# Optimization experiments

Measured on AMD Instinct MI355X. Metric: run time of the kernel, lower is better.

The kernel has to match this reference:

```python
import jax, jax.numpy as jnp
import numpy as np

B, IN, HID, LAT, EH = 32768, 512, 2048, 128, 512
MID = max(HID // 2, LAT * 2)      # 1024
HALF = max(EH // 2, 4)            # 256
EPS = 1e-5
LN10 = float(np.log(10.0))


def setup_inputs() -> dict:
    key = jax.random.key(0)
    ks = jax.random.split(key, 24)
    r = lambda k, shp, s=0.02: (jax.random.normal(k, shp, dtype=jnp.float32) * s)
    d = {
        "x": jax.random.normal(ks[0], (B, IN), dtype=jnp.float32),
        "group_idx": jax.random.randint(ks[1], (B,), 0, 3),
        # encoder: Linear(IN,HID)+BN+ELU, Linear(HID,MID)+BN+ELU, Linear(MID,LAT)
        "e_w1": r(ks[2], (HID, IN)), "e_b1": jnp.zeros((HID,), jnp.float32),
        "e_g1": jnp.ones((HID,), jnp.float32), "e_be1": jnp.zeros((HID,), jnp.float32),
        "e_w2": r(ks[3], (MID, HID)), "e_b2": jnp.zeros((MID,), jnp.float32),
        "e_g2": jnp.ones((MID,), jnp.float32), "e_be2": jnp.zeros((MID,), jnp.float32),
        "e_w3": r(ks[4], (LAT, MID)), "e_b3": jnp.zeros((LAT,), jnp.float32),
        # shared: Linear(LAT+IN,HID)+BN+ELU, Linear(HID,MID)+BN+ELU
        "s_w1": r(ks[5], (HID, LAT + IN)), "s_b1": jnp.zeros((HID,), jnp.float32),
        "s_g1": jnp.ones((HID,), jnp.float32), "s_be1": jnp.zeros((HID,), jnp.float32),
        "s_w2": r(ks[6], (MID, HID)), "s_b2": jnp.zeros((MID,), jnp.float32),
        "s_g2": jnp.ones((MID,), jnp.float32), "s_be2": jnp.zeros((MID,), jnp.float32),
        # 3 expert heads, stacked on leading axis E=3
        "h_w1": r(ks[7], (3, EH, MID)), "h_b1": jnp.zeros((3, EH), jnp.float32),
        "h_w2": r(ks[8], (3, HALF, EH)), "h_b2": jnp.zeros((3, HALF), jnp.float32),
        "h_w3": r(ks[9], (3, HALF)), "h_b3": jnp.zeros((3,), jnp.float32),
    }
    return d


def _bn(h, g, b):
    # BatchNorm1d in training mode: batch mean, biased batch var
    m = jnp.mean(h, axis=0)
    v = jnp.var(h, axis=0)
    return (h - m) * (g / jnp.sqrt(v + EPS)) + b


def _elu(h):
    return jax.nn.elu(h)


def reference(x, group_idx,
              e_w1, e_b1, e_g1, e_be1, e_w2, e_b2, e_g2, e_be2, e_w3, e_b3,
              s_w1, s_b1, s_g1, s_be1, s_w2, s_b2, s_g2, s_be2,
              h_w1, h_b1, h_w2, h_b2, h_w3, h_b3):
    # encoder
    h = _elu(_bn(x @ e_w1.T + e_b1, e_g1, e_be1))
    h = _elu(_bn(h @ e_w2.T + e_b2, e_g2, e_be2))
    latent = h @ e_w3.T + e_b3                              # [B, LAT]
    # shared trunk
    z = jnp.concatenate([latent, x], axis=-1)               # [B, LAT+IN]
    h = _elu(_bn(z @ s_w1.T + s_b1, s_g1, s_be1))
    hidden = _elu(_bn(h @ s_w2.T + s_b2, s_g2, s_be2))      # [B, MID]
    # expert heads: compute all 3 (tiny vs trunk), then select per-row group
    t1 = _elu(jnp.einsum('bm,ehm->ebh', hidden, h_w1) + h_b1[:, None, :])   # [3,B,EH]
    t2 = _elu(jnp.einsum('ebh,efh->ebf', t1, h_w2) + h_b2[:, None, :])      # [3,B,HALF]
    pred_all = jnp.einsum('ebf,ef->eb', t2, h_w3) + h_b3[:, None]           # [3,B]
    pred_raw = jnp.take_along_axis(pred_all, group_idx[None, :], axis=0)[0] # [B]
    pred_log = -jax.nn.softplus(pred_raw)
    pred_prob = jnp.exp(pred_log * jnp.float32(LN10))       # 10 ** pred_log
    return pred_log, pred_prob
```

## Files before the change

### kernel.cpp

```cpp
#include <hip/hip_runtime.h>
#include <math.h>

#define B_    32768
#define LN10_ 2.302585092994046f
#define MT_H  264
#define NBLK  128

typedef __attribute__((ext_vector_type(8))) short short8;
typedef __attribute__((ext_vector_type(4))) float f32x4;

typedef const __attribute__((address_space(1))) void gvoid_t;
typedef __attribute__((address_space(3))) void svoid_t;

__device__ __forceinline__ void gl16(const void* g, void* l) {
  __builtin_amdgcn_global_load_lds((gvoid_t*)g, (svoid_t*)l, 16, 0, 0);
}

__device__ __forceinline__ float bf2f(unsigned int u) {
  union { unsigned int i; float f; } v; v.i = u << 16; return v.f;
}
__device__ __forceinline__ unsigned short f2bf(float f) {
  union { float f; unsigned int i; } v; v.f = f;
  unsigned int x = v.i;
  unsigned int r = x + 0x7FFFu + ((x >> 16) & 1u);
  return (unsigned short)(r >> 16);
}

#define HLF 8192

__global__ __launch_bounds__(512)
void gemm256(const unsigned short* __restrict__ A0_, int lda,
             const unsigned short* __restrict__ W0_, int ldw,
             unsigned short* __restrict__ C0, int ldc, int K,
             float* __restrict__ st, int Ntot) {
  __shared__ __align__(16) unsigned short lds[65536];
  const int t = threadIdx.x;
  const int nx = gridDim.x, ny = gridDim.y;
  const int f = blockIdx.y * nx + blockIdx.x;
  const int xcd = f & 7, g = f >> 3;
  const int gdiv = g / nx;
  const int mt = xcd * (ny >> 3) + gdiv;
  const int nt = g - gdiv * nx;
  const int mBase = mt * 256, nBase = nt * 256;
  const unsigned short* Ap = A0_ + (size_t)mBase * lda;
  const unsigned short* Wp = W0_ + (size_t)nBase * ldw;
  const int w = t >> 6, l = t & 63;
  const int wr = w >> 2, wc = w & 3;
  const int lm = l & 15, lg = l >> 4;

  const int rr = t >> 3;
  const int xc = ((t & 7) ^ (rr & 7)) << 3;
  const unsigned short* gA = Ap + (size_t)rr * lda + xc;
  const unsigned short* gB = Wp + (size_t)rr * ldw + xc;

#define SG(ptr, ld, rowoff, dst) \
    gl16((ptr) + (size_t)(rowoff) * (ld) + ko_, &lds[(dst) + t * 8])
#define STAGE_A0(tt) { const int d_=((tt)&1)<<15; const size_t ko_=(size_t)(tt)*64; \
    SG(gA,lda,0,d_);          SG(gA,lda,64,d_+4096); }
#define STAGE_A1(tt) { const int d_=((tt)&1)<<15; const size_t ko_=(size_t)(tt)*64; \
    SG(gA,lda,128,d_+8192);   SG(gA,lda,192,d_+12288); }
#define STAGE_B0(tt) { const int d_=((tt)&1)<<15; const size_t ko_=(size_t)(tt)*64; \
    SG(gB,ldw,0,d_+16384);    SG(gB,ldw,64,d_+20480); }
#define STAGE_B1(tt) { const int d_=((tt)&1)<<15; const size_t ko_=(size_t)(tt)*64; \
    SG(gB,ldw,128,d_+24576);  SG(gB,ldw,192,d_+28672); }

  const int cs0 = ((lg) ^ (l & 7)) << 3;
  const int cs1 = ((4 | lg) ^ (l & 7)) << 3;

  f32x4 acc[8][4];
#pragma unroll
  for (int i = 0; i < 8; ++i)
#pragma unroll
    for (int j = 0; j < 4; ++j) {
      f32x4 z4 = {0.f, 0.f, 0.f, 0.f};
      acc[i][j] = z4;
    }

  const int NT = K >> 6;
  STAGE_A0(0); STAGE_A1(0); STAGE_B0(0); STAGE_B1(0);
  asm volatile("s_waitcnt vmcnt(2)" ::: "memory");
  __builtin_amdgcn_s_barrier();

  short8 af[8], bq[4];
  for (int tt = 0; tt < NT; ++tt) {
    const int d = (tt & 1) << 15;
    const bool more = (tt + 1 < NT);
    const int abase = d + wr * HLF + lm * 64;
    const int bbase = d + 2 * HLF + (wc * 32 + lm) * 64;
#pragma unroll
    for (int i = 0; i < 8; ++i) af[i] = *(const short8*)&lds[abase + i * 1024 + cs0];
    bq[0] = *(const short8*)&lds[bbase + cs0];
    bq[1] = *(const short8*)&lds[bbase + 1024 + cs0];
    if (more) {
      STAGE_A0(tt + 1);
      asm volatile("s_waitcnt vmcnt(2)" ::: "memory");
    } else {
      asm volatile("s_waitcnt vmcnt(0)" ::: "memory");
    }
    __builtin_amdgcn_s_barrier();
    asm volatile("s_waitcnt lgkmcnt(0)" ::: "memory");
    __builtin_amdgcn_sched_barrier(0);
    __builtin_amdgcn_s_setprio(1);
#pragma unroll
    for (int i = 0; i < 8; ++i) {
      acc[i][0] = __builtin_amdgcn_mfma_f32_16x16x32_bf16(af[i], bq[0], acc[i][0], 0, 0, 0);
      acc[i][1] = __builtin_amdgcn_mfma_f32_16x16x32_bf16(af[i], bq[1], acc[i][1], 0, 0, 0);
    }
    __builtin_amdgcn_s_setprio(0);
    __builtin_amdgcn_s_barrier();
    bq[2] = *(const short8*)&lds[bbase + HLF + cs0];
    bq[3] = *(const short8*)&lds[bbase + HLF + 1024 + cs0];
    if (more) STAGE_A1(tt + 1);
    __builtin_amdgcn_s_barrier();
    asm volatile("s_waitcnt lgkmcnt(0)" ::: "memory");
    __builtin_amdgcn_sched_barrier(0);
    __builtin_amdgcn_s_setprio(1);
#pragma unroll
    for (int i = 0; i < 8; ++i) {
      acc[i][2] = __builtin_amdgcn_mfma_f32_16x16x32_bf16(af[i], bq[2], acc[i][2], 0, 0, 0);
      acc[i][3] = __builtin_amdgcn_mfma_f32_16x16x32_bf16(af[i], bq[3], acc[i][3], 0, 0, 0);
    }
    __builtin_amdgcn_s_setprio(0);
    __builtin_amdgcn_s_barrier();
#pragma unroll
    for (int i = 0; i < 8; ++i) af[i] = *(const short8*)&lds[abase + i * 1024 + cs1];
    bq[0] = *(const short8*)&lds[bbase + cs1];
    bq[1] = *(const short8*)&lds[bbase + 1024 + cs1];
    if (more) STAGE_B0(tt + 1);
    __builtin_amdgcn_s_barrier();
    asm volatile("s_waitcnt lgkmcnt(0)" ::: "memory");
    __builtin_amdgcn_sched_barrier(0);
    __builtin_amdgcn_s_setprio(1);
#pragma unroll
    for (int i = 0; i < 8; ++i) {
      acc[i][0] = __builtin_amdgcn_mfma_f32_16x16x32_bf16(af[i], bq[0], acc[i][0], 0, 0, 0);
      acc[i][1] = __builtin_amdgcn_mfma_f32_16x16x32_bf16(af[i], bq[1], acc[i][1], 0, 0, 0);
    }
    __builtin_amdgcn_s_setprio(0);
    __builtin_amdgcn_s_barrier();
    bq[2] = *(const short8*)&lds[bbase + HLF + cs1];
    bq[3] = *(const short8*)&lds[bbase + HLF + 1024 + cs1];
    if (more) {
      STAGE_B1(tt + 1);
      asm volatile("s_waitcnt vmcnt(2)" ::: "memory");
    }
    __builtin_amdgcn_s_barrier();
    asm volatile("s_waitcnt lgkmcnt(0)" ::: "memory");
    __builtin_amdgcn_sched_barrier(0);
    __builtin_amdgcn_s_setprio(1);
#pragma unroll
    for (int i = 0; i < 8; ++i) {
      acc[i][2] = __builtin_amdgcn_mfma_f32_16x16x32_bf16(af[i], bq[2], acc[i][2], 0, 0, 0);
      acc[i][3] = __builtin_amdgcn_mfma_f32_16x16x32_bf16(af[i], bq[3], acc[i][3], 0, 0, 0);
    }
    __builtin_amdgcn_s_setprio(0);
    __builtin_amdgcn_s_barrier();
  }

#pragma unroll
  for (int j = 0; j < 4; ++j) {
    int n = nBase + (j >> 1) * 128 + wc * 32 + (j & 1) * 16 + lm;
    float s1 = 0.f, q1 = 0.f;
#pragma unroll
    for (int i = 0; i < 8; ++i) {
      int m0 = mBase + wr * 128 + i * 16 + lg * 4;
#pragma unroll
      for (int r = 0; r < 4; ++r) {
        float v = acc[i][j][r];
        s1 += v; q1 += v * v;
        C0[(size_t)(m0 + r) * ldc + n] = f2bf(v);
      }
    }
    s1 += __shfl_xor(s1, 16, 64); s1 += __shfl_xor(s1, 32, 64);
    q1 += __shfl_xor(q1, 16, 64); q1 += __shfl_xor(q1, 32, 64);
    if (lg == 0) { atomicAdd(&st[n], s1); atomicAdd(&st[Ntot + n], q1); }
  }
}
#undef SG
#undef STAGE_A0
#undef STAGE_A1
#undef STAGE_B0
#undef STAGE_B1

__global__ __launch_bounds__(256)
void gemm_bt(const unsigned short* __restrict__ A0, int lda,
             const unsigned short* __restrict__ W0, int ldw,
             unsigned short* __restrict__ C0, int ldc,
             int K, const float* __restrict__ bias0, int elu,
             float* __restrict__ st, int Ntot,
             long eA, long eW, long eC, int eBias,
             const int* __restrict__ texp) {
  __shared__ __align__(16) unsigned short lA[128 * 64];
  __shared__ __align__(16) unsigned short lB[128 * 64];
  const int t = threadIdx.x;
  const int nx = gridDim.x, ny = gridDim.y;
  const int f = blockIdx.y * nx + blockIdx.x;
  const int xcd = f & 7, g = f >> 3;
  const int gdiv = g / nx;
  const int mt = xcd * (ny >> 3) + gdiv;
  const int nt = g - gdiv * nx;
  const int mBase = mt * 128;
  const int nBase = nt * 128;
  int e = texp ? texp[mt] : (int)blockIdx.z;
  if (e < 0) return;
  const unsigned short* A = A0 + (size_t)e * eA;
  const unsigned short* W = W0 + (size_t)e * eW;
  unsigned short* C = C0 + (size_t)e * eC;
  const float* bias = bias0 ? (bias0 + (size_t)e * eBias) : nullptr;
  const unsigned short* Ap = A + (size_t)mBase * lda;
  const unsigned short* Wp = W + (size_t)nBase * ldw;
  const int w = t >> 6, l = t & 63;
  const int wr = (w >> 1) * 64, wc = (w & 1) * 64;
  const int lm = l & 15, lg = l >> 4;

  f32x4 acc[4][4];
#pragma unroll
  for (int i = 0; i < 4; ++i)
#pragma unroll
    for (int j = 0; j < 4; ++j) {
      f32x4 z4 = {0.f, 0.f, 0.f, 0.f};
      acc[i][j] = z4;
    }

  for (int k0 = 0; k0 < K; k0 += 64) {
    __syncthreads();
#pragma unroll
    for (int it = 0; it < 4; ++it) {
      int chunk = it * 256 + t;
      int row = chunk >> 3, sc = chunk & 7;
      int gc = (sc ^ (row & 7)) << 3;
      gl16(Ap + (size_t)row * lda + k0 + gc, &lA[chunk * 8]);
      gl16(Wp + (size_t)row * ldw + k0 + gc, &lB[chunk * 8]);
    }
    __syncthreads();
#pragma unroll
    for (int kk = 0; kk < 64; kk += 32) {
      short8 af[4], bfr[4];
#pragma unroll
      for (int i = 0; i < 4; ++i) {
        int ar = wr + i * 16 + lm;
        int ac = (kk >> 3) + lg;
        af[i] = *(const short8*)&lA[ar * 64 + ((ac ^ (ar & 7)) << 3)];
      }
#pragma unroll
      for (int j = 0; j < 4; ++j) {
        int br = wc + j * 16 + lm;
        int bc = (kk >> 3) + lg;
        bfr[j] = *(const short8*)&lB[br * 64 + ((bc ^ (br & 7)) << 3)];
      }
#pragma unroll
      for (int i = 0; i < 4; ++i)
#pragma unroll
        for (int j = 0; j < 4; ++j)
          acc[i][j] = __builtin_amdgcn_mfma_f32_16x16x32_bf16(af[i], bfr[j], acc[i][j], 0, 0, 0);
    }
  }

#pragma unroll
  for (int j = 0; j < 4; ++j) {
    int n = nBase + wc + j * 16 + lm;
    float bj = bias ? bias[n] : 0.f;
    float s = 0.f, q = 0.f;
#pragma unroll
    for (int i = 0; i < 4; ++i) {
      int m0 = mBase + wr + i * 16 + lg * 4;
#pragma unroll
      for (int r = 0; r < 4; ++r) {
        float v = acc[i][j][r] + bj;
        if (elu) v = v > 0.f ? v : expm1f(v);
        s += v; q += v * v;
        C[(size_t)(m0 + r) * ldc + n] = f2bf(v);
      }
    }
    if (st) {
      s += __shfl_xor(s, 16, 64); s += __shfl_xor(s, 32, 64);
      q += __shfl_xor(q, 16, 64); q += __shfl_xor(q, 32, 64);
      if (lg == 0) { atomicAdd(&st[n], s); atomicAdd(&st[Ntot + n], q); }
    }
  }
}

__global__ void bn_apply(unsigned short* __restrict__ Y, const float* __restrict__ st,
                         const float* __restrict__ gam, const float* __restrict__ bet,
                         int N, float invB) {
  size_t i = (size_t)blockIdx.x * blockDim.x + threadIdx.x;
  size_t base = i * 8;
  int col = (int)(base & (size_t)(N - 1));
  float a8[8], b8[8];
#pragma unroll
  for (int k = 0; k < 8; ++k) {
    int c = col + k;
    float m = st[c] * invB;
    float var = st[N + c] * invB - m * m;
    float av = gam[c] * rsqrtf(var + 1e-5f);
    a8[k] = av;
    b8[k] = bet[c] - m * av;
  }
  uint4 u = *(uint4*)&Y[base];
  unsigned int uu[4] = {u.x, u.y, u.z, u.w};
  unsigned int oo[4];
#pragma unroll
  for (int k = 0; k < 4; ++k) {
    float vlo = bf2f(uu[k] & 0xFFFFu);
    float vhi = bf2f(uu[k] >> 16);
    float flo = a8[2 * k] * vlo + b8[2 * k];
    float fhi = a8[2 * k + 1] * vhi + b8[2 * k + 1];
    flo = flo > 0.f ? flo : expm1f(flo);
    fhi = fhi > 0.f ? fhi : expm1f(fhi);
    oo[k] = (unsigned int)f2bf(flo) | ((unsigned int)f2bf(fhi) << 16);
  }
  uint4 o = {oo[0], oo[1], oo[2], oo[3]};
  *(uint4*)&Y[base] = o;
}

__global__ void cast_all(const float* __restrict__ e1, const float* __restrict__ e2,
                         const float* __restrict__ e3, const float* __restrict__ s1,
                         const float* __restrict__ s2, const float* __restrict__ h1,
                         const float* __restrict__ h2, unsigned short* __restrict__ dst) {
  int i4 = blockIdx.x * 256 + threadIdx.x;
  const float* src;
  int rel;
  if (i4 < 786432) {
    if (i4 < 262144) { src = e1; rel = i4; }
    else             { src = e2; rel = i4 - 262144; }
  } else if (i4 < 1146880) {
    if (i4 < 819200) { src = e3; rel = i4 - 786432; }
    else             { src = s1; rel = i4 - 819200; }
  } else if (i4 < 2064384) {
    if (i4 < 1671168) { src = s2; rel = i4 - 1146880; }
    else              { src = h1; rel = i4 - 1671168; }
  } else { src = h2; rel = i4 - 2064384; }
  float4 v = ((const float4*)src)[rel];
  ushort4 o = {f2bf(v.x), f2bf(v.y), f2bf(v.z), f2bf(v.w)};
  ((ushort4*)dst)[i4] = o;
}

__global__ void cast_x(const float* __restrict__ x, unsigned short* __restrict__ z) {
  int i = blockIdx.x * blockDim.x + threadIdx.x;
  int b = i >> 7;
  int c = (i & 127) << 2;
  float4 v = *(const float4*)&x[(size_t)b * 512 + c];
  ushort4 o = {f2bf(v.x), f2bf(v.y), f2bf(v.z), f2bf(v.w)};
  *(ushort4*)&z[(size_t)b * 640 + 128 + c] = o;
}

__global__ void hist_blocks(const int* __restrict__ gidx, int* __restrict__ bcnt) {
  int blk = blockIdx.x;
  int i = blk * 256 + threadIdx.x;
  int e = gidx[i];
  int l = threadIdx.x & 63, w = threadIdx.x >> 6;
  __shared__ int wc[4][3];
  unsigned long long m0 = __ballot(e == 0);
  unsigned long long m1 = __ballot(e == 1);
  unsigned long long m2 = __ballot(e == 2);
  if (l == 0) { wc[w][0] = __popcll(m0); wc[w][1] = __popcll(m1); wc[w][2] = __popcll(m2); }
  __syncthreads();
  if (threadIdx.x < 3)
    bcnt[blk * 3 + threadIdx.x] = wc[0][threadIdx.x] + wc[1][threadIdx.x] +
                                  wc[2][threadIdx.x] + wc[3][threadIdx.x];
}

__global__ void scan_plan(const int* __restrict__ bcnt, int* __restrict__ boff,
                          int* __restrict__ vend, int* __restrict__ texp) {
  __shared__ int sp[4];
  __shared__ int cnt[3];
  int t = threadIdx.x;
  if (t < 3) {
    int s = 0;
    for (int b = 0; b < NBLK; ++b) s += bcnt[b * 3 + t];
    cnt[t] = s;
  }
  __syncthreads();
  if (t == 0) {
    int p = 0;
    for (int e = 0; e < 3; ++e) {
      sp[e] = p; vend[e] = p + cnt[e];
      p += ((cnt[e] + 127) >> 7) << 7;
    }
    sp[3] = p;
  }
  __syncthreads();
  if (t < 3) {
    int run = sp[t];
    for (int b = 0; b < NBLK; ++b) { boff[b * 3 + t] = run; run += bcnt[b * 3 + t]; }
  }
  if (t < MT_H) {
    int r0 = t << 7, e = -1;
    for (int k = 0; k < 3; ++k)
      if (r0 >= sp[k] && r0 < sp[k + 1]) e = k;
    texp[t] = e;
  }
}

__global__ void scatter2(const int* __restrict__ gidx, const int* __restrict__ boff,
                         int* __restrict__ perm) {
  int blk = blockIdx.x;
  int i = blk * 256 + threadIdx.x;
  int e = gidx[i];
  int l = threadIdx.x & 63, w = threadIdx.x >> 6;
  __shared__ int wc[4][3];
  unsigned long long m0 = __ballot(e == 0);
  unsigned long long m1 = __ballot(e == 1);
  unsigned long long m2 = __ballot(e == 2);
  if (l == 0) { wc[w][0] = __popcll(m0); wc[w][1] = __popcll(m1); wc[w][2] = __popcll(m2); }
  __syncthreads();
  unsigned long long me = (e == 0) ? m0 : ((e == 1) ? m1 : m2);
  int rank = __popcll(me & ((1ull << l) - 1ull));
  int woff = 0;
  for (int ww = 0; ww < w; ++ww) woff += wc[ww][e];
  perm[boff[blk * 3 + e] + woff + rank] = i;
}

__global__ void gather_bn(const unsigned short* __restrict__ hid, const int* __restrict__ perm,
                          const int* __restrict__ texp, const int* __restrict__ vend,
                          const float* __restrict__ st, const float* __restrict__ gam,
                          const float* __restrict__ bet, float invB,
                          unsigned short* __restrict__ ht) {
  int idx = blockIdx.x * 256 + threadIdx.x;
  int p = idx >> 7, c8 = (idx & 127) << 3;
  int e = texp[p >> 7];
  uint4 o = {0u, 0u, 0u, 0u};
  if (e >= 0 && p < vend[e]) {
    float a8[8], b8[8];
#pragma unroll
    for (int k = 0; k < 8; ++k) {
      int c = c8 + k;
      float m = st[c] * invB;
      float var = st[1024 + c] * invB - m * m;
      float av = gam[c] * rsqrtf(var + 1e-5f);
      a8[k] = av;
      b8[k] = bet[c] - m * av;
    }
    int src = perm[p];
    uint4 u = *(const uint4*)&hid[(size_t)src * 1024 + c8];
    unsigned int uu[4] = {u.x, u.y, u.z, u.w};
    unsigned int oo[4];
#pragma unroll
    for (int k = 0; k < 4; ++k) {
      float vlo = bf2f(uu[k] & 0xFFFFu);
      float vhi = bf2f(uu[k] >> 16);
      float flo = a8[2 * k] * vlo + b8[2 * k];
      float fhi = a8[2 * k + 1] * vhi + b8[2 * k + 1];
      flo = flo > 0.f ? flo : expm1f(flo);
      fhi = fhi > 0.f ? fhi : expm1f(fhi);
      oo[k] = (unsigned int)f2bf(flo) | ((unsigned int)f2bf(fhi) << 16);
    }
    o.x = oo[0]; o.y = oo[1]; o.z = oo[2]; o.w = oo[3];
  }
  *(uint4*)&ht[(size_t)p * 1024 + c8] = o;
}

__global__ void final_pred(const unsigned short* __restrict__ t2, const int* __restrict__ perm,
                           const int* __restrict__ texp, const int* __restrict__ vend,
                           const float* __restrict__ w3, const float* __restrict__ b3,
                           float* __restrict__ out) {
  int p = blockIdx.x * 4 + (threadIdx.x >> 6);
  int l = threadIdx.x & 63;
  int e = texp[p >> 7];
  if (e < 0 || p >= vend[e]) return;
  ushort4 u = *(const ushort4*)&t2[(size_t)p * 256 + l * 4];
  float4 wv = *(const float4*)&w3[e * 256 + l * 4];
  float sum = bf2f(u.x) * wv.x + bf2f(u.y) * wv.y + bf2f(u.z) * wv.z + bf2f(u.w) * wv.w;
#pragma unroll
  for (int off = 32; off; off >>= 1) sum += __shfl_down(sum, off, 64);
  if (l == 0) {
    int orig = perm[p];
    float xr = sum + b3[e];
    float sp = (xr > 0.f) ? (xr + log1pf(expf(-xr))) : log1pf(expf(xr));
    float pl = -sp;
    out[orig] = pl;
    out[B_ + orig] = expf(pl * LN10_);
  }
}

extern "C" void kernel_launch(void* const* d_in, const int* in_sizes, int n_in,
                              void* d_out, int out_size, void* d_ws, size_t ws_size,
                              hipStream_t stream) {
  const float* x    = (const float*)d_in[0];
  const int*   gidx = (const int*)d_in[1];
  const float* e_w1 = (const float*)d_in[2];
  const float* e_g1 = (const float*)d_in[4];
  const float* e_be1= (const float*)d_in[5];
  const float* e_w2 = (const float*)d_in[6];
  const float* e_g2 = (const float*)d_in[8];
  const float* e_be2= (const float*)d_in[9];
  const float* e_w3 = (const float*)d_in[10];
  const float* e_b3 = (const float*)d_in[11];
  const float* s_w1 = (const float*)d_in[12];
  const float* s_g1 = (const float*)d_in[14];
  const float* s_be1= (const float*)d_in[15];
  const float* s_w2 = (const float*)d_in[16];
  const float* s_g2 = (const float*)d_in[18];
  const float* s_be2= (const float*)d_in[19];
  const float* h_w1 = (const float*)d_in[20];
  const float* h_b1 = (const float*)d_in[21];
  const float* h_w2 = (const float*)d_in[22];
  const float* h_b2 = (const float*)d_in[23];
  const float* h_w3 = (const float*)d_in[24];
  const float* h_b3 = (const float*)d_in[25];
  float* out = (float*)d_out;

  char* ws = (char*)d_ws;
  size_t off = 0;
  auto alloc = [&](size_t bytes) -> char* {
    char* p = ws + off;
    off += (bytes + 255) & ~(size_t)255;
    return p;
  };
  unsigned short* wb_e1 = (unsigned short*)alloc((size_t)2048 * 512 * 2);
  unsigned short* wb_e2 = (unsigned short*)alloc((size_t)1024 * 2048 * 2);
  unsigned short* wb_e3 = (unsigned short*)alloc((size_t)128 * 1024 * 2);
  unsigned short* wb_s1 = (unsigned short*)alloc((size_t)2048 * 640 * 2);
  unsigned short* wb_s2 = (unsigned short*)alloc((size_t)1024 * 2048 * 2);
  unsigned short* wb_h1 = (unsigned short*)alloc((size_t)3 * 512 * 1024 * 2);
  unsigned short* wb_h2 = (unsigned short*)alloc((size_t)3 * 256 * 512 * 2);
  unsigned short* z     = (unsigned short*)alloc((size_t)B_ * 640 * 2);
  unsigned short* bufA  = (unsigned short*)alloc((size_t)B_ * 2048 * 2);
  unsigned short* bufB  = (unsigned short*)alloc((size_t)B_ * 1024 * 2);
  float* st = (float*)alloc(12288 * sizeof(float));
  float* st0 = st;
  float* st1 = st + 4096;
  float* st2 = st + 6144;
  float* st3 = st + 10240;
  int* bcnt = (int*)alloc(NBLK * 3 * sizeof(int));
  int* boff = (int*)alloc(NBLK * 3 * sizeof(int));
  int* vend = (int*)alloc(3 * sizeof(int));
  int* texp = (int*)alloc(MT_H * sizeof(int));
  int* perm = (int*)alloc((size_t)MT_H * 128 * sizeof(int));
  unsigned short* ht  = bufA;
  unsigned short* t1p = bufA + (size_t)MT_H * 128 * 1024;
  unsigned short* t2p = z;

  cast_all<<<8448, 256, 0, stream>>>(e_w1, e_w2, e_w3, s_w1, s_w2, h_w1, h_w2, wb_e1);
  cast_x<<<(B_ * 128) / 256, 256, 0, stream>>>(x, z);
  hipMemsetAsync(st, 0, 12288 * sizeof(float), stream);
  hist_blocks<<<NBLK, 256, 0, stream>>>(gidx, bcnt);
  scan_plan<<<1, 512, 0, stream>>>(bcnt, boff, vend, texp);
  scatter2<<<NBLK, 256, 0, stream>>>(gidx, boff, perm);

  gemm256<<<dim3(8, 128), 512, 0, stream>>>(z + 128, 640, wb_e1, 512, bufA, 2048, 512,
                                            st0, 2048);
  bn_apply<<<B_, 256, 0, stream>>>(bufA, st0, e_g1, e_be1, 2048, 1.0f / B_);
  gemm256<<<dim3(4, 128), 512, 0, stream>>>(bufA, 2048, wb_e2, 2048, bufB, 1024, 2048,
                                            st1, 1024);
  bn_apply<<<B_ / 2, 256, 0, stream>>>(bufB, st1, e_g2, e_be2, 1024, 1.0f / B_);
  gemm_bt<<<dim3(1, 256), 256, 0, stream>>>(bufB, 1024, wb_e3, 1024, z, 640, 1024,
                                            e_b3, 0, nullptr, 0, 0, 0, 0, 0, nullptr);
  gemm256<<<dim3(8, 128), 512, 0, stream>>>(z, 640, wb_s1, 640, bufA, 2048, 640,
                                            st2, 2048);
  bn_apply<<<B_, 256, 0, stream>>>(bufA, st2, s_g1, s_be1, 2048, 1.0f / B_);
  gemm256<<<dim3(4, 128), 512, 0, stream>>>(bufA, 2048, wb_s2, 2048, bufB, 1024, 2048,
                                            st3, 1024);

  gather_bn<<<(MT_H * 128 * 128) / 256, 256, 0, stream>>>(bufB, perm, texp, vend,
                                                          st3, s_g2, s_be2, 1.0f / B_, ht);

  gemm_bt<<<dim3(4, MT_H), 256, 0, stream>>>(ht, 1024, wb_h1, 1024, t1p, 512, 1024,
                                             h_b1, 1, nullptr, 0,
                                             0, (long)512 * 1024, 0, 512, texp);
  gemm_bt<<<dim3(2, MT_H), 256, 0, stream>>>(t1p, 512, wb_h2, 512, t2p, 256, 512,
                                             h_b2, 1, nullptr, 0,
                                             0, (long)256 * 512, 0, 256, texp);

  final_pred<<<(MT_H * 128) / 4, 256, 0, stream>>>(t2p, perm, texp, vend, h_w3, h_b3, out);
}
```

Baseline: 955.4 us.

## Fuse BN+ELU of HID layers into the following GEMM's A-operand load

Removes the two standalone bn_apply passes over the B×2048 activations. A small kernel now precomputes per-channel scale and shift, and a new GEMM variant applies affine+ELU while staging A into LDS. A is loaded through registers instead of direct global-to-LDS copies. This saves a full read and write of the 128MB intermediate twice but adds ALU and expm1 work, plus register pressure inside the GEMM's main loop.

```diff
diff --git a/kernel.cpp b/kernel.cpp
--- a/kernel.cpp
+++ b/kernel.cpp
@@ -181,6 +181,170 @@
 #undef STAGE_A1
 #undef STAGE_B0
 #undef STAGE_B1
+
+__global__ __launch_bounds__(512)
+void gemm256f(const unsigned short* __restrict__ A0_, int lda,
+              const unsigned short* __restrict__ W0_, int ldw,
+              unsigned short* __restrict__ C0, int ldc, int K,
+              float* __restrict__ stOut, int Ntot,
+              const float* __restrict__ coef) {
+  __shared__ __align__(16) unsigned short lds[65536];
+  const int t = threadIdx.x;
+  const int nx = gridDim.x, ny = gridDim.y;
+  const int f = blockIdx.y * nx + blockIdx.x;
+  const int xcd = f & 7, g = f >> 3;
+  const int gdiv = g / nx;
+  const int mt = xcd * (ny >> 3) + gdiv;
+  const int nt = g - gdiv * nx;
+  const int mBase = mt * 256, nBase = nt * 256;
+  const unsigned short* Ap = A0_ + (size_t)mBase * lda;
+  const unsigned short* Wp = W0_ + (size_t)nBase * ldw;
+  const int w = t >> 6, l = t & 63;
+  const int wr = w >> 2, wc = w & 3;
+  const int lm = l & 15, lg = l >> 4;
+
+  const int rr = t >> 3;
+  const int c8 = (t & 7) << 3;
+  const int swz = ((t & 7) ^ (rr & 7)) << 3;
+  const unsigned short* gAf = Ap + (size_t)rr * lda + c8;
+  const unsigned short* gB  = Wp + (size_t)rr * ldw + swz;
+
+#define FSTAGE_B(tt) { const int d_=((tt)&1)<<15; const size_t ko_=(size_t)(tt)*64; \
+    gl16(gB + ko_,                     &lds[d_ + 16384 + t * 8]);  \
+    gl16(gB + (size_t)64  * ldw + ko_, &lds[d_ + 20480 + t * 8]);  \
+    gl16(gB + (size_t)128 * ldw + ko_, &lds[d_ + 24576 + t * 8]);  \
+    gl16(gB + (size_t)192 * ldw + ko_, &lds[d_ + 28672 + t * 8]); }
+
+  uint4 ar0, ar1, ar2, ar3;
+  float4 caLo, caHi, cbLo, cbHi;
+#define FLOADA(tt) { const size_t ko_ = (size_t)(tt) * 64; const int cb_ = (tt) * 64 + c8; \
+    ar0 = *(const uint4*)&gAf[ko_];                        \
+    ar1 = *(const uint4*)&gAf[(size_t)64  * lda + ko_];    \
+    ar2 = *(const uint4*)&gAf[(size_t)128 * lda + ko_];    \
+    ar3 = *(const uint4*)&gAf[(size_t)192 * lda + ko_];    \
+    caLo = *(const float4*)&coef[cb_];     caHi = *(const float4*)&coef[cb_ + 4];     \
+    cbLo = *(const float4*)&coef[K + cb_]; cbHi = *(const float4*)&coef[K + cb_ + 4]; }
+
+  const int cs0 = ((lg) ^ (l & 7)) << 3;
+  const int cs1 = ((4 | lg) ^ (l & 7)) << 3;
+
+  f32x4 acc[8][4];
+#pragma unroll
+  for (int i = 0; i < 8; ++i)
+#pragma unroll
+    for (int j = 0; j < 4; ++j) {
+      f32x4 z4 = {0.f, 0.f, 0.f, 0.f};
+      acc[i][j] = z4;
+    }
+
+  const int NT = K >> 6;
+  FLOADA(0); FSTAGE_B(0);
+
+  for (int tt = 0; tt < NT; ++tt) {
+    const int d = (tt & 1) << 15;
+    asm volatile("s_waitcnt vmcnt(0)" ::: "memory");
+    __builtin_amdgcn_sched_barrier(0);
+    {
+      float a8[8] = {caLo.x, caLo.y, caLo.z, caLo.w, caHi.x, caHi.y, caHi.z, caHi.w};
+      float b8[8] = {cbLo.x, cbLo.y, cbLo.z, cbLo.w, cbHi.x, cbHi.y, cbHi.z, cbHi.w};
+      uint4 uregs[4] = {ar0, ar1, ar2, ar3};
+#pragma unroll
+      for (int r2 = 0; r2 < 4; ++r2) {
+        unsigned int uu[4] = {uregs[r2].x, uregs[r2].y, uregs[r2].z, uregs[r2].w};
+        unsigned int oo[4];
+#pragma unroll
+        for (int k2 = 0; k2 < 4; ++k2) {
+          float vlo = bf2f(uu[k2] & 0xFFFFu);
+          float vhi = bf2f(uu[k2] >> 16);
+          float flo = a8[2 * k2] * vlo + b8[2 * k2];
+          float fhi = a8[2 * k2 + 1] * vhi + b8[2 * k2 + 1];
+          flo = flo > 0.f ? flo : expm1f(flo);
+          fhi = fhi > 0.f ? fhi : expm1f(fhi);
+          oo[k2] = (unsigned int)f2bf(flo) | ((unsigned int)f2bf(fhi) << 16);
+        }
+        uint4 ov = {oo[0], oo[1], oo[2], oo[3]};
+        *(uint4*)&lds[d + ((r2 * 64 + rr) << 6) + swz] = ov;
+      }
+    }
+    const bool more = (tt + 1 < NT);
+    if (more) { FLOADA(tt + 1); FSTAGE_B(tt + 1); }
+    asm volatile("s_waitcnt lgkmcnt(0)" ::: "memory");
+    __builtin_amdgcn_s_barrier();
+    __builtin_amdgcn_sched_barrier(0);
+    {
+      short8 af[8], bq[4];
+#pragma unroll
+      for (int i = 0; i < 8; ++i) {
+        int arow = wr * 128 + i * 16 + lm;
+        af[i] = *(const short8*)&lds[d + arow * 64 + cs0];
+      }
+#pragma unroll
+      for (int j = 0; j < 4; ++j) {
+        int brow = wc * 64 + j * 16 + lm;
+        bq[j] = *(const short8*)&lds[d + 16384 + brow * 64 + cs0];
+      }
+      __builtin_amdgcn_s_setprio(1);
+#pragma unroll
+      for (int i = 0; i < 8; ++i)
+#pragma unroll
+        for (int j = 0; j < 4; ++j)
+          acc[i][j] = __builtin_amdgcn_mfma_f32_16x16x32_bf16(af[i], bq[j], acc[i][j], 0, 0, 0);
+      __builtin_amdgcn_s_setprio(0);
+    }
+    {
+      short8 af[8], bq[4];
+#pragma unroll
+      for (int i = 0; i < 8; ++i) {
+        int arow = wr * 128 + i * 16 + lm;
+        af[i] = *(const short8*)&lds[d + arow * 64 + cs1];
+      }
+#pragma unroll
+      for (int j = 0; j < 4; ++j) {
+        int brow = wc * 64 + j * 16 + lm;
+        bq[j] = *(const short8*)&lds[d + 16384 + brow * 64 + cs1];
+      }
+      __builtin_amdgcn_s_setprio(1);
+#pragma unroll
+      for (int i = 0; i < 8; ++i)
+#pragma unroll
+        for (int j = 0; j < 4; ++j)
+          acc[i][j] = __builtin_amdgcn_mfma_f32_16x16x32_bf16(af[i], bq[j], acc[i][j], 0, 0, 0);
+      __builtin_amdgcn_s_setprio(0);
+    }
+  }
+
+#pragma unroll
+  for (int j = 0; j < 4; ++j) {
+    int n = nBase + wc * 64 + j * 16 + lm;
+    float s1 = 0.f, q1 = 0.f;
+#pragma unroll
+    for (int i = 0; i < 8; ++i) {
+      int m0 = mBase + wr * 128 + i * 16 + lg * 4;
+#pragma unroll
+      for (int r = 0; r < 4; ++r) {
+        float v = acc[i][j][r];
+        s1 += v; q1 += v * v;
+        C0[(size_t)(m0 + r) * ldc + n] = f2bf(v);
+      }
+    }
+    s1 += __shfl_xor(s1, 16, 64); s1 += __shfl_xor(s1, 32, 64);
+    q1 += __shfl_xor(q1, 16, 64); q1 += __shfl_xor(q1, 32, 64);
+    if (lg == 0) { atomicAdd(&stOut[n], s1); atomicAdd(&stOut[Ntot + n], q1); }
+  }
+}
+#undef FSTAGE_B
+#undef FLOADA
+
+__global__ void bn_coef(const float* __restrict__ st, const float* __restrict__ gam,
+                        const float* __restrict__ bet, float* __restrict__ coef,
+                        int N, float invB) {
+  int c = blockIdx.x * 256 + threadIdx.x;
+  float m = st[c] * invB;
+  float var = st[N + c] * invB - m * m;
+  float av = gam[c] * rsqrtf(var + 1e-5f);
+  coef[c] = av;
+  coef[N + c] = bet[c] - m * av;
+}
 
 __global__ __launch_bounds__(256)
 void gemm_bt(const unsigned short* __restrict__ A0, int lda,
@@ -522,6 +686,7 @@
   float* st1 = st + 4096;
   float* st2 = st + 6144;
   float* st3 = st + 10240;
+  float* coefbuf = (float*)alloc(4096 * sizeof(float));
   int* bcnt = (int*)alloc(NBLK * 3 * sizeof(int));
   int* boff = (int*)alloc(NBLK * 3 * sizeof(int));
   int* vend = (int*)alloc(3 * sizeof(int));
@@ -540,17 +705,17 @@
 
   gemm256<<<dim3(8, 128), 512, 0, stream>>>(z + 128, 640, wb_e1, 512, bufA, 2048, 512,
                                             st0, 2048);
-  bn_apply<<<B_, 256, 0, stream>>>(bufA, st0, e_g1, e_be1, 2048, 1.0f / B_);
-  gemm256<<<dim3(4, 128), 512, 0, stream>>>(bufA, 2048, wb_e2, 2048, bufB, 1024, 2048,
-                                            st1, 1024);
+  bn_coef<<<8, 256, 0, stream>>>(st0, e_g1, e_be1, coefbuf, 2048, 1.0f / B_);
+  gemm256f<<<dim3(4, 128), 512, 0, stream>>>(bufA, 2048, wb_e2, 2048, bufB, 1024, 2048,
+                                             st1, 1024, coefbuf);
   bn_apply<<<B_ / 2, 256, 0, stream>>>(bufB, st1, e_g2, e_be2, 1024, 1.0f / B_);
   gemm_bt<<<dim3(1, 256), 256, 0, stream>>>(bufB, 1024, wb_e3, 1024, z, 640, 1024,
                                             e_b3, 0, nullptr, 0, 0, 0, 0, 0, nullptr);
   gemm256<<<dim3(8, 128), 512, 0, stream>>>(z, 640, wb_s1, 640, bufA, 2048, 640,
                                             st2, 2048);
-  bn_apply<<<B_, 256, 0, stream>>>(bufA, st2, s_g1, s_be1, 2048, 1.0f / B_);
-  gemm256<<<dim3(4, 128), 512, 0, stream>>>(bufA, 2048, wb_s2, 2048, bufB, 1024, 2048,
-                                            st3, 1024);
+  bn_coef<<<8, 256, 0, stream>>>(st2, s_g1, s_be1, coefbuf, 2048, 1.0f / B_);
+  gemm256f<<<dim3(4, 128), 512, 0, stream>>>(bufA, 2048, wb_s2, 2048, bufB, 1024, 2048,
+                                             st3, 1024, coefbuf);
 
   gather_bn<<<(MT_H * 128 * 128) / 256, 256, 0, stream>>>(bufB, perm, texp, vend,
                                                           st3, s_g2, s_be2, 1.0f / B_, ht);
```

After: 1.184 ms. +23.9%, slower.

## Restructure gemm256 mainloop into deeper prefetch with full-K fragment loads

Applied to the files above, without the earlier changes.

Reworks the 256x256 GEMM main loop so each phase loads both K-halves of A/B fragments and runs paired MFMAs over half the M rows. Global-to-LDS staging is reordered to prefetch two tiles ahead for some sub-tiles, with vmcnt waits adjusted to match. Several per-phase barriers are removed. The goal is fewer barriers and better overlap of memory with MFMA work. The cost is more complex buffer-reuse hazards inside the double-buffered LDS.

```diff
diff --git a/kernel.cpp b/kernel.cpp
--- a/kernel.cpp
+++ b/kernel.cpp
@@ -25,8 +25,6 @@
   unsigned int r = x + 0x7FFFu + ((x >> 16) & 1u);
   return (unsigned short)(r >> 16);
 }
-
-#define HLF 8192
 
 __global__ __launch_bounds__(512)
 void gemm256(const unsigned short* __restrict__ A0_, int lda,
@@ -55,10 +53,10 @@
 
 #define SG(ptr, ld, rowoff, dst) \
     gl16((ptr) + (size_t)(rowoff) * (ld) + ko_, &lds[(dst) + t * 8])
-#define STAGE_A0(tt) { const int d_=((tt)&1)<<15; const size_t ko_=(size_t)(tt)*64; \
-    SG(gA,lda,0,d_);          SG(gA,lda,64,d_+4096); }
-#define STAGE_A1(tt) { const int d_=((tt)&1)<<15; const size_t ko_=(size_t)(tt)*64; \
-    SG(gA,lda,128,d_+8192);   SG(gA,lda,192,d_+12288); }
+#define STAGE_Aa(tt) { const int d_=((tt)&1)<<15; const size_t ko_=(size_t)(tt)*64; \
+    SG(gA,lda,0,d_);          SG(gA,lda,128,d_+8192); }
+#define STAGE_Ab(tt) { const int d_=((tt)&1)<<15; const size_t ko_=(size_t)(tt)*64; \
+    SG(gA,lda,64,d_+4096);    SG(gA,lda,192,d_+12288); }
 #define STAGE_B0(tt) { const int d_=((tt)&1)<<15; const size_t ko_=(size_t)(tt)*64; \
     SG(gB,ldw,0,d_+16384);    SG(gB,ldw,64,d_+20480); }
 #define STAGE_B1(tt) { const int d_=((tt)&1)<<15; const size_t ko_=(size_t)(tt)*64; \
@@ -77,84 +75,97 @@
     }
 
   const int NT = K >> 6;
-  STAGE_A0(0); STAGE_A1(0); STAGE_B0(0); STAGE_B1(0);
-  asm volatile("s_waitcnt vmcnt(2)" ::: "memory");
+  STAGE_Aa(0); STAGE_B0(0); STAGE_B1(0); STAGE_Ab(0);
+  if (NT > 1) {
+    STAGE_Aa(1); STAGE_B0(1); STAGE_B1(1);
+    asm volatile("s_waitcnt vmcnt(6)" ::: "memory");
+  } else {
+    asm volatile("s_waitcnt vmcnt(0)" ::: "memory");
+  }
   __builtin_amdgcn_s_barrier();
-
-  short8 af[8], bq[4];
+  __builtin_amdgcn_sched_barrier(0);
+
+  short8 af[4][2], b01[2][2], b23[2][2];
   for (int tt = 0; tt < NT; ++tt) {
     const int d = (tt & 1) << 15;
-    const bool more = (tt + 1 < NT);
-    const int abase = d + wr * HLF + lm * 64;
-    const int bbase = d + 2 * HLF + (wc * 32 + lm) * 64;
-#pragma unroll
-    for (int i = 0; i < 8; ++i) af[i] = *(const short8*)&lds[abase + i * 1024 + cs0];
-    bq[0] = *(const short8*)&lds[bbase + cs0];
-    bq[1] = *(const short8*)&lds[bbase + 1024 + cs0];
-    if (more) {
-      STAGE_A0(tt + 1);
-      asm volatile("s_waitcnt vmcnt(2)" ::: "memory");
-    } else {
-      asm volatile("s_waitcnt vmcnt(0)" ::: "memory");
-    }
+    const int abase = d + (wr * 128 + lm) * 64;
+    const int bbase = d + 16384 + (wc * 32 + lm) * 64;
+    const bool s1ok = (tt + 1 < NT), s2ok = (tt + 2 < NT);
+#pragma unroll
+    for (int fi = 0; fi < 4; ++fi) {
+      af[fi][0] = *(const short8*)&lds[abase + fi * 1024 + cs0];
+      af[fi][1] = *(const short8*)&lds[abase + fi * 1024 + cs1];
+    }
+#pragma unroll
+    for (int fj = 0; fj < 2; ++fj) {
+      b01[fj][0] = *(const short8*)&lds[bbase + fj * 1024 + cs0];
+      b01[fj][1] = *(const short8*)&lds[bbase + fj * 1024 + cs1];
+    }
+    if (s1ok) STAGE_Ab(tt + 1);
     __builtin_amdgcn_s_barrier();
     asm volatile("s_waitcnt lgkmcnt(0)" ::: "memory");
     __builtin_amdgcn_sched_barrier(0);
     __builtin_amdgcn_s_setprio(1);
 #pragma unroll
-    for (int i = 0; i < 8; ++i) {
-      acc[i][0] = __builtin_amdgcn_mfma_f32_16x16x32_bf16(af[i], bq[0], acc[i][0], 0, 0, 0);
-      acc[i][1] = __builtin_amdgcn_mfma_f32_16x16x32_bf16(af[i], bq[1], acc[i][1], 0, 0, 0);
+    for (int fi = 0; fi < 4; ++fi) {
+      acc[fi][0] = __builtin_amdgcn_mfma_f32_16x16x32_bf16(af[fi][0], b01[0][0], acc[fi][0], 0, 0, 0);
+      acc[fi][0] = __builtin_amdgcn_mfma_f32_16x16x32_bf16(af[fi][1], b01[0][1], acc[fi][0], 0, 0, 0);
+      acc[fi][1] = __builtin_amdgcn_mfma_f32_16x16x32_bf16(af[fi][0], b01[1][0], acc[fi][1], 0, 0, 0);
+      acc[fi][1] = __builtin_amdgcn_mfma_f32_16x16x32_bf16(af[fi][1], b01[1][1], acc[fi][1], 0, 0, 0);
     }
     __builtin_amdgcn_s_setprio(0);
-    __builtin_amdgcn_s_barrier();
-    bq[2] = *(const short8*)&lds[bbase + HLF + cs0];
-    bq[3] = *(const short8*)&lds[bbase + HLF + 1024 + cs0];
-    if (more) STAGE_A1(tt + 1);
+#pragma unroll
+    for (int fj = 0; fj < 2; ++fj) {
+      b23[fj][0] = *(const short8*)&lds[bbase + 8192 + fj * 1024 + cs0];
+      b23[fj][1] = *(const short8*)&lds[bbase + 8192 + fj * 1024 + cs1];
+    }
+    if (s2ok) STAGE_Aa(tt + 2);
     __builtin_amdgcn_s_barrier();
     asm volatile("s_waitcnt lgkmcnt(0)" ::: "memory");
     __builtin_amdgcn_sched_barrier(0);
     __builtin_amdgcn_s_setprio(1);
 #pragma unroll
-    for (int i = 0; i < 8; ++i) {
-      acc[i][2] = __builtin_amdgcn_mfma_f32_16x16x32_bf16(af[i], bq[2], acc[i][2], 0, 0, 0);
-      acc[i][3] = __builtin_amdgcn_mfma_f32_16x16x32_bf16(af[i], bq[3], acc[i][3], 0, 0, 0);
+    for (int fi = 0; fi < 4; ++fi) {
+      acc[fi][2] = __builtin_amdgcn_mfma_f32_16x16x32_bf16(af[fi][0], b23[0][0], acc[fi][2], 0, 0, 0);
+      acc[fi][2] = __builtin_amdgcn_mfma_f32_16x16x32_bf16(af[fi][1], b23[0][1], acc[fi][2], 0, 0, 0);
+      acc[fi][3] = __builtin_amdgcn_mfma_f32_16x16x32_bf16(af[fi][0], b23[1][0], acc[fi][3], 0, 0, 0);
+      acc[fi][3] = __builtin_amdgcn_mfma_f32_16x16x32_bf16(af[fi][1], b23[1][1], acc[fi][3], 0, 0, 0);
     }
     __builtin_amdgcn_s_setprio(0);
-    __builtin_amdgcn_s_barrier();
-#pragma unroll
-    for (int i = 0; i < 8; ++i) af[i] = *(const short8*)&lds[abase + i * 1024 + cs1];
-    bq[0] = *(const short8*)&lds[bbase + cs1];
-    bq[1] = *(const short8*)&lds[bbase + 1024 + cs1];
-    if (more) STAGE_B0(tt + 1);
+#pragma unroll
+    for (int fi = 0; fi < 4; ++fi) {
+      af[fi][0] = *(const short8*)&lds[abase + 4096 + fi * 1024 + cs0];
+      af[fi][1] = *(const short8*)&lds[abase + 4096 + fi * 1024 + cs1];
+    }
+    if (s2ok) STAGE_B0(tt + 2);
     __builtin_amdgcn_s_barrier();
     asm volatile("s_waitcnt lgkmcnt(0)" ::: "memory");
     __builtin_amdgcn_sched_barrier(0);
     __builtin_amdgcn_s_setprio(1);
 #pragma unroll
-    for (int i = 0; i < 8; ++i) {
-      acc[i][0] = __builtin_amdgcn_mfma_f32_16x16x32_bf16(af[i], bq[0], acc[i][0], 0, 0, 0);
-      acc[i][1] = __builtin_amdgcn_mfma_f32_16x16x32_bf16(af[i], bq[1], acc[i][1], 0, 0, 0);
+    for (int fi = 0; fi < 4; ++fi) {
+      acc[4 + fi][0] = __builtin_amdgcn_mfma_f32_16x16x32_bf16(af[fi][0], b01[0][0], acc[4 + fi][0], 0, 0, 0);
+      acc[4 + fi][0] = __builtin_amdgcn_mfma_f32_16x16x32_bf16(af[fi][1], b01[0][1], acc[4 + fi][0], 0, 0, 0);
+      acc[4 + fi][1] = __builtin_amdgcn_mfma_f32_16x16x32_bf16(af[fi][0], b01[1][0], acc[4 + fi][1], 0, 0, 0);
+      acc[4 + fi][1] = __builtin_amdgcn_mfma_f32_16x16x32_bf16(af[fi][1], b01[1][1], acc[4 + fi][1], 0, 0, 0);
     }
     __builtin_amdgcn_s_setprio(0);
-    __builtin_amdgcn_s_barrier();
-    bq[2] = *(const short8*)&lds[bbase + HLF + cs1];
-    bq[3] = *(const short8*)&lds[bbase + HLF + 1024 + cs1];
-    if (more) {
-      STAGE_B1(tt + 1);
-      asm volatile("s_waitcnt vmcnt(2)" ::: "memory");
-    }
-    __builtin_amdgcn_s_barrier();
-    asm volatile("s_waitcnt lgkmcnt(0)" ::: "memory");
-    __builtin_amdgcn_sched_barrier(0);
+    if (s2ok) STAGE_B1(tt + 2);
     __builtin_amdgcn_s_setprio(1);
 #pragma unroll
-    for (int i = 0; i < 8; ++i) {
-      acc[i][2] = __builtin_amdgcn_mfma_f32_16x16x32_bf16(af[i], bq[2], acc[i][2], 0, 0, 0);
-      acc[i][3] = __builtin_amdgcn_mfma_f32_16x16x32_bf16(af[i], bq[3], acc[i][3], 0, 0, 0);
+    for (int fi = 0; fi < 4; ++fi) {
+      acc[4 + fi][2] = __builtin_amdgcn_mfma_f32_16x16x32_bf16(af[fi][0], b23[0][0], acc[4 + fi][2], 0, 0, 0);
+      acc[4 + fi][2] = __builtin_amdgcn_mfma_f32_16x16x32_bf16(af[fi][1], b23[0][1], acc[4 + fi][2], 0, 0, 0);
+      acc[4 + fi][3] = __builtin_amdgcn_mfma_f32_16x16x32_bf16(af[fi][0], b23[1][0], acc[4 + fi][3], 0, 0, 0);
+      acc[4 + fi][3] = __builtin_amdgcn_mfma_f32_16x16x32_bf16(af[fi][1], b23[1][1], acc[4 + fi][3], 0, 0, 0);
     }
     __builtin_amdgcn_s_setprio(0);
-    __builtin_amdgcn_s_barrier();
+    if (s1ok) {
+      if (s2ok) { asm volatile("s_waitcnt vmcnt(6)" ::: "memory"); }
+      else      { asm volatile("s_waitcnt vmcnt(0)" ::: "memory"); }
+      __builtin_amdgcn_s_barrier();
+      __builtin_amdgcn_sched_barrier(0);
+    }
   }
 
 #pragma unroll
@@ -177,8 +188,8 @@
   }
 }
 #undef SG
-#undef STAGE_A0
-#undef STAGE_A1
+#undef STAGE_Aa
+#undef STAGE_Ab
 #undef STAGE_B0
 #undef STAGE_B1
 
```

After: 940.1 us. Within noise of the previous version (-1.6%).
